# Kernel tuning notes

Measured on AMD Instinct MI355X. Metric: run time of the kernel, lower is better.

The kernel has to match this reference:

```python
import jax, jax.numpy as jnp
import numpy as np


def setup_inputs() -> dict:
    key = jax.random.key(0)
    ks = jax.random.split(key, 7)
    B, N, F, H = 128, 64, 128, 128
    s1 = 1.0 / np.sqrt(2 * N)  # torch Linear default-ish scaling
    s2 = 1.0 / np.sqrt(H)
    return {
        "agent_features": jax.random.normal(ks[0], (B, N, F), dtype=jnp.float32),
        "W1": jax.random.normal(ks[1], (2 * N, H), dtype=jnp.float32) * s1,
        "b1": jax.random.normal(ks[2], (H,), dtype=jnp.float32) * s1,
        "W2": jax.random.normal(ks[3], (H, H), dtype=jnp.float32) * s2,
        "b2": jax.random.normal(ks[4], (H,), dtype=jnp.float32) * s2,
        "w3": jax.random.normal(ks[5], (H,), dtype=jnp.float32) * s2,
        "b3": jax.random.normal(ks[6], (1,), dtype=jnp.float32) * s2,
        "mixing_weights": jnp.ones((N,), dtype=jnp.float32) / N,
    }


def reference(agent_features, W1, b1, W2, b2, w3, b3, mixing_weights):
    N = mixing_weights.shape[0]
    f = agent_features[:, :, :N]  # [B, N, N] (first num_agents features)
    # Split first Linear's weight into the i-half and j-half of the concat:
    # concat([f_i, f_j]) @ W1 == f_i @ W1[:N] + f_j @ W1[N:]
    Ai = jnp.einsum('bnf,fh->bnh', f, W1[:N])   # contribution of agent i
    Aj = jnp.einsum('bnf,fh->bnh', f, W1[N:])   # contribution of agent j
    h1 = jax.nn.relu(Ai[:, :, None, :] + Aj[:, None, :, :] + b1)  # [B,N,N,H]
    h2 = jax.nn.relu(jnp.einsum('bijh,hk->bijk', h1, W2) + b2)    # [B,N,N,H]
    correlations = jax.nn.sigmoid(jnp.einsum('bijh,h->bij', h2, w3) + b3[0])
    weights = jax.nn.softmax(mixing_weights, axis=0)
    return correlations, weights
```

## Files before the change

kernel.cpp:

```cpp
#include <hip/hip_runtime.h>
#include <hip/hip_bf16.h>


typedef __bf16 bf16x8 __attribute__((ext_vector_type(8)));
typedef float f32x4 __attribute__((ext_vector_type(4)));
typedef float f32x2 __attribute__((ext_vector_type(2)));

#define B_SZ 128
#define N_SZ 64
#define H_SZ 128

union Frag16 {
  uint4 q;
  __hip_bfloat162 h[4];
};

__global__ __launch_bounds__(256) void setup_kernel(
    const float* __restrict__ af, const float* __restrict__ W1,
    const float* __restrict__ b1, const float* __restrict__ W2,
    const float* __restrict__ mw, float* __restrict__ AiP,
    float* __restrict__ Aj, unsigned short* __restrict__ W2T,
    float* __restrict__ outw)
{
  const int blk = blockIdx.x;
  const int tid = threadIdx.x;

  if (blk < 2048) {
    __shared__ float fl[4 * 64];
    const int bn0 = blk << 2;
    fl[tid] = af[((bn0 + (tid >> 6)) << 7) + (tid & 63)];
    __syncthreads();
    const int h    = tid & 127;
    const int half = tid >> 7;
    const float* Wp = W1 + ((half << 6) << 7) + h;
    float acc0 = 0.f, acc1 = 0.f, acc2 = 0.f, acc3 = 0.f;
#pragma unroll
    for (int fq = 0; fq < 16; ++fq) {
      const float w0 = Wp[(fq * 4 + 0) << 7];
      const float w1v = Wp[(fq * 4 + 1) << 7];
      const float w2v = Wp[(fq * 4 + 2) << 7];
      const float w3v = Wp[(fq * 4 + 3) << 7];
      const float4 f0 = *(const float4*)&fl[0 * 64 + (fq << 2)];
      const float4 f1 = *(const float4*)&fl[1 * 64 + (fq << 2)];
      const float4 f2 = *(const float4*)&fl[2 * 64 + (fq << 2)];
      const float4 f3 = *(const float4*)&fl[3 * 64 + (fq << 2)];
      acc0 = fmaf(f0.x, w0, fmaf(f0.y, w1v, fmaf(f0.z, w2v, fmaf(f0.w, w3v, acc0))));
      acc1 = fmaf(f1.x, w0, fmaf(f1.y, w1v, fmaf(f1.z, w2v, fmaf(f1.w, w3v, acc1))));
      acc2 = fmaf(f2.x, w0, fmaf(f2.y, w1v, fmaf(f2.z, w2v, fmaf(f2.w, w3v, acc2))));
      acc3 = fmaf(f3.x, w0, fmaf(f3.y, w1v, fmaf(f3.z, w2v, fmaf(f3.w, w3v, acc3))));
    }
    if (half == 0) {
      const float bb = b1[h];
      AiP[((bn0 + 0) << 7) + h] = acc0 + bb;
      AiP[((bn0 + 1) << 7) + h] = acc1 + bb;
      AiP[((bn0 + 2) << 7) + h] = acc2 + bb;
      AiP[((bn0 + 3) << 7) + h] = acc3 + bb;
    } else {
      Aj[((bn0 + 0) << 7) + h] = acc0;
      Aj[((bn0 + 1) << 7) + h] = acc1;
      Aj[((bn0 + 2) << 7) + h] = acc2;
      Aj[((bn0 + 3) << 7) + h] = acc3;
    }
  } else if (blk < 2112) {
    int idx = ((blk - 2048) << 8) + tid;
    int k = idx >> 7, n = idx & 127;
    unsigned u = __float_as_uint(W2[idx]);
    u += 0x7fffu + ((u >> 16) & 1u);
    W2T[(n << 7) + k] = (unsigned short)(u >> 16);
  } else {
    if (tid < 64) {
      float v = mw[tid];
      float m = v;
      for (int off = 32; off > 0; off >>= 1) m = fmaxf(m, __shfl_xor(m, off));
      float e = expf(v - m);
      float s = e;
      for (int off = 32; off > 0; off >>= 1) s += __shfl_xor(s, off);
      outw[tid] = e / s;
    }
  }
}

__global__ __launch_bounds__(512, 4) void corr_kernel(
    const float* __restrict__ AiP, const float* __restrict__ Aj,
    const unsigned short* __restrict__ W2T,
    const float* __restrict__ b2, const float* __restrict__ w3,
    const float* __restrict__ b3, float* __restrict__ out)
{
  __shared__ __align__(16) unsigned short W2s[128 * 128];
  __shared__ __align__(16) unsigned short At[128 * 128];
  __shared__ float part[256];

  const int tid  = threadIdx.x;
  const int lane = tid & 63;
  const int wave = tid >> 6;
  const int c = lane & 15, g = lane >> 4;
  const int wm = wave & 1;
  const int wn = wave >> 1;

  const int blk = blockIdx.x;
  const int b   = blk >> 2;
  const int ip0 = (blk & 3) << 3;

  {
    const uint4* src = (const uint4*)W2T;
#pragma unroll
    for (int it = 0; it < 4; ++it) {
      const int idx = (it << 9) + tid;
      const int n = idx >> 4, e = idx & 15;
      const uint4 v = src[idx];
      *(uint4*)&W2s[(n << 7) + ((e ^ (n & 15)) << 3)] = v;
    }
  }

  f32x4 b2v[4], w3v[4];
#pragma unroll
  for (int tm = 0; tm < 4; ++tm) {
    b2v[tm] = *(const f32x4*)(b2 + (wm << 6) + (tm << 4) + (g << 2));
    w3v[tm] = *(const f32x4*)(w3 + (wm << 6) + (tm << 4) + (g << 2));
  }
  const float bias3 = b3[0];
  const f32x4 zero4 = {0.f, 0.f, 0.f, 0.f};
  const f32x2 zero2 = {0.f, 0.f};

  const float* AjB = Aj + ((b << 6) << 7);

  const int kq8 = tid & 15;
  const int rr  = tid >> 4;

  for (int t = 0; t < 8; ++t) {
    const int i0 = (ip0 + t) << 1;
    const float* AiB = AiP + (((b << 6) + i0) << 7);

#pragma unroll
    for (int pass = 0; pass < 4; ++pass) {
      const int r = (pass << 5) + rr;
      const float* arow = AiB + ((r >> 6) << 7) + (kq8 << 3);
      const float* jrow = AjB + ((r & 63) << 7) + (kq8 << 3);
      const f32x4 a0 = *(const f32x4*)arow;
      const f32x4 a1 = *(const f32x4*)(arow + 4);
      const f32x4 j0 = *(const f32x4*)jrow;
      const f32x4 j1 = *(const f32x4*)(jrow + 4);
      const f32x4 s0 = __builtin_elementwise_max(a0 + j0, zero4);
      const f32x4 s1 = __builtin_elementwise_max(a1 + j1, zero4);
      Frag16 u;
      u.h[0] = __float22bfloat162_rn(float2{s0.x, s0.y});
      u.h[1] = __float22bfloat162_rn(float2{s0.z, s0.w});
      u.h[2] = __float22bfloat162_rn(float2{s1.x, s1.y});
      u.h[3] = __float22bfloat162_rn(float2{s1.z, s1.w});
      *(uint4*)&At[(r << 7) + ((kq8 ^ (r & 15)) << 3)] = u.q;
    }

    __syncthreads();

    f32x4 acc[4][2];
#pragma unroll
    for (int tm = 0; tm < 4; ++tm) {
      acc[tm][0] = b2v[tm];
      acc[tm][1] = b2v[tm];
    }

#pragma unroll
    for (int kt = 0; kt < 4; ++kt) {
      const int es = ((kt << 2) + g) ^ c;
      bf16x8 wv[4], hv[2];
#pragma unroll
      for (int tm = 0; tm < 4; ++tm)
        wv[tm] = *(const bf16x8*)&W2s[(((wm << 6) + (tm << 4) + c) << 7) + (es << 3)];
#pragma unroll
      for (int tn = 0; tn < 2; ++tn)
        hv[tn] = *(const bf16x8*)&At[(((wn << 5) + (tn << 4) + c) << 7) + (es << 3)];
#pragma unroll
      for (int tm = 0; tm < 4; ++tm)
#pragma unroll
        for (int tn = 0; tn < 2; ++tn)
          acc[tm][tn] = __builtin_amdgcn_mfma_f32_16x16x32_bf16(
              wv[tm], hv[tn], acc[tm][tn], 0, 0, 0);
    }

    f32x2 sp0 = zero2, sp1 = zero2;
#pragma unroll
    for (int tm = 0; tm < 4; ++tm) {
      const f32x2 w3a = w3v[tm].xy, w3b = w3v[tm].zw;
      sp0 = __builtin_elementwise_max(acc[tm][0].xy, zero2) * w3a + sp0;
      sp0 = __builtin_elementwise_max(acc[tm][0].zw, zero2) * w3b + sp0;
      sp1 = __builtin_elementwise_max(acc[tm][1].xy, zero2) * w3a + sp1;
      sp1 = __builtin_elementwise_max(acc[tm][1].zw, zero2) * w3b + sp1;
    }
    float s0 = sp0.x + sp0.y;
    float s1 = sp1.x + sp1.y;
    s0 += __shfl_xor(s0, 16);
    s0 += __shfl_xor(s0, 32);
    s1 += __shfl_xor(s1, 16);
    s1 += __shfl_xor(s1, 32);
    if (g == 0) {
      part[(((wn << 5) + c) << 1) + wm]      = s0;
      part[(((wn << 5) + 16 + c) << 1) + wm] = s1;
    }

    __syncthreads();

    if (tid < 128) {
      const float2 pp = *(const float2*)&part[tid << 1];
      const float v = pp.x + pp.y + bias3;
      out[(b << 12) + (i0 << 6) + tid] = 1.f / (1.f + __expf(-v));
    }
  }
}

extern "C" void kernel_launch(void* const* d_in, const int* in_sizes, int n_in,
                              void* d_out, int out_size, void* d_ws,
                              size_t ws_size, hipStream_t stream)
{
  const float* af = (const float*)d_in[0];
  const float* W1 = (const float*)d_in[1];
  const float* b1 = (const float*)d_in[2];
  const float* W2 = (const float*)d_in[3];
  const float* b2 = (const float*)d_in[4];
  const float* w3 = (const float*)d_in[5];
  const float* b3 = (const float*)d_in[6];
  const float* mw = (const float*)d_in[7];
  float* out = (float*)d_out;

  float* AiP = (float*)d_ws;
  float* Aj  = AiP + B_SZ * N_SZ * H_SZ;
  unsigned short* W2T = (unsigned short*)(Aj + B_SZ * N_SZ * H_SZ);

  setup_kernel<<<2113, 256, 0, stream>>>(af, W1, b1, W2, mw, AiP, Aj, W2T,
                                         out + B_SZ * N_SZ * N_SZ);
  corr_kernel<<<512, 512, 0, stream>>>(AiP, Aj, W2T, b2, w3, b3, out);
}
```

Measured before the change: 103.7 us.

## Keep W2 in registers and double-buffer h1 tiles in corr kernel

The correlation kernel now holds its W2 fragments in registers, loaded once per block, instead of staging W2 in shared memory. Blocks shrink to 256 threads handling one i-row per step, and the h1 tile for the next step is built into a second shared buffer while the current one feeds the MFMAs. The grid doubles to 1024 blocks. b2 and w3 are copied by the setup kernel into a small table read each step, which trims register use at the cost of extra loads per iteration. The intent is to remove the per-block W2 shared-memory fill and LDS reads of W2, and to overlap building h1 with compute. In exchange, the 64 extra VGPRs for W2 could limit occupancy.

```diff
diff --git a/kernel.cpp b/kernel.cpp
--- a/kernel.cpp
+++ b/kernel.cpp
@@ -18,9 +18,10 @@
 __global__ __launch_bounds__(256) void setup_kernel(
     const float* __restrict__ af, const float* __restrict__ W1,
     const float* __restrict__ b1, const float* __restrict__ W2,
-    const float* __restrict__ mw, float* __restrict__ AiP,
+    const float* __restrict__ mw, const float* __restrict__ b2,
+    const float* __restrict__ w3, float* __restrict__ AiP,
     float* __restrict__ Aj, unsigned short* __restrict__ W2T,
-    float* __restrict__ outw)
+    float* __restrict__ tab, float* __restrict__ outw)
 {
   const int blk = blockIdx.x;
   const int tid = threadIdx.x;
@@ -67,7 +68,7 @@
     unsigned u = __float_as_uint(W2[idx]);
     u += 0x7fffu + ((u >> 16) & 1u);
     W2T[(n << 7) + k] = (unsigned short)(u >> 16);
-  } else {
+  } else if (blk == 2112) {
     if (tid < 64) {
       float v = mw[tid];
       float m = v;
@@ -77,18 +78,20 @@
       for (int off = 32; off > 0; off >>= 1) s += __shfl_xor(s, off);
       outw[tid] = e / s;
     }
+  } else {
+    const float v = (tid < 128) ? b2[tid] : w3[tid - 128];
+    tab[tid] = v;
+    tab[tid + 256] = v;
   }
 }
 
-__global__ __launch_bounds__(512, 4) void corr_kernel(
+__global__ __launch_bounds__(256, 4) void corr_kernel(
     const float* __restrict__ AiP, const float* __restrict__ Aj,
-    const unsigned short* __restrict__ W2T,
-    const float* __restrict__ b2, const float* __restrict__ w3,
+    const unsigned short* __restrict__ W2T, const float* __restrict__ tab,
     const float* __restrict__ b3, float* __restrict__ out)
 {
-  __shared__ __align__(16) unsigned short W2s[128 * 128];
-  __shared__ __align__(16) unsigned short At[128 * 128];
-  __shared__ float part[256];
+  __shared__ __align__(16) unsigned short S[2][64 * 128];
+  __shared__ float part[2][128];
 
   const int tid  = threadIdx.x;
   const int lane = tid & 63;
@@ -97,49 +100,34 @@
   const int wm = wave & 1;
   const int wn = wave >> 1;
 
-  const int blk = blockIdx.x;
-  const int b   = blk >> 2;
-  const int ip0 = (blk & 3) << 3;
-
-  {
-    const uint4* src = (const uint4*)W2T;
-#pragma unroll
-    for (int it = 0; it < 4; ++it) {
-      const int idx = (it << 9) + tid;
-      const int n = idx >> 4, e = idx & 15;
-      const uint4 v = src[idx];
-      *(uint4*)&W2s[(n << 7) + ((e ^ (n & 15)) << 3)] = v;
-    }
-  }
-
-  f32x4 b2v[4], w3v[4];
-#pragma unroll
-  for (int tm = 0; tm < 4; ++tm) {
-    b2v[tm] = *(const f32x4*)(b2 + (wm << 6) + (tm << 4) + (g << 2));
-    w3v[tm] = *(const f32x4*)(w3 + (wm << 6) + (tm << 4) + (g << 2));
-  }
+  const int b  = blockIdx.x >> 3;
+  const int i0 = (blockIdx.x & 7) << 3;
+
+  bf16x8 wv[4][4];
+#pragma unroll
+  for (int tm = 0; tm < 4; ++tm)
+#pragma unroll
+    for (int kt = 0; kt < 4; ++kt)
+      wv[tm][kt] = *(const bf16x8*)&W2T[(((wm << 6) + (tm << 4) + c) << 7) +
+                                        (((kt << 2) + g) << 3)];
+
+  const float* AjB = Aj + ((b << 6) << 7);
+  const int kq8 = tid & 15;
+  const int rr  = tid >> 4;
   const float bias3 = b3[0];
   const f32x4 zero4 = {0.f, 0.f, 0.f, 0.f};
   const f32x2 zero2 = {0.f, 0.f};
 
-  const float* AjB = Aj + ((b << 6) << 7);
-
-  const int kq8 = tid & 15;
-  const int rr  = tid >> 4;
-
-  for (int t = 0; t < 8; ++t) {
-    const int i0 = (ip0 + t) << 1;
-    const float* AiB = AiP + (((b << 6) + i0) << 7);
-
+  {
+    const float* AiB = AiP + (((b << 6) + i0) << 7) + (kq8 << 3);
+    const f32x4 a0 = *(const f32x4*)AiB;
+    const f32x4 a1 = *(const f32x4*)(AiB + 4);
 #pragma unroll
     for (int pass = 0; pass < 4; ++pass) {
-      const int r = (pass << 5) + rr;
-      const float* arow = AiB + ((r >> 6) << 7) + (kq8 << 3);
-      const float* jrow = AjB + ((r & 63) << 7) + (kq8 << 3);
-      const f32x4 a0 = *(const f32x4*)arow;
-      const f32x4 a1 = *(const f32x4*)(arow + 4);
-      const f32x4 j0 = *(const f32x4*)jrow;
-      const f32x4 j1 = *(const f32x4*)(jrow + 4);
+      const int r = (pass << 4) + rr;
+      const float* jr = AjB + (r << 7) + (kq8 << 3);
+      const f32x4 j0 = *(const f32x4*)jr;
+      const f32x4 j1 = *(const f32x4*)(jr + 4);
       const f32x4 s0 = __builtin_elementwise_max(a0 + j0, zero4);
       const f32x4 s1 = __builtin_elementwise_max(a1 + j1, zero4);
       Frag16 u;
@@ -147,44 +135,50 @@
       u.h[1] = __float22bfloat162_rn(float2{s0.z, s0.w});
       u.h[2] = __float22bfloat162_rn(float2{s1.x, s1.y});
       u.h[3] = __float22bfloat162_rn(float2{s1.z, s1.w});
-      *(uint4*)&At[(r << 7) + ((kq8 ^ (r & 15)) << 3)] = u.q;
-    }
-
-    __syncthreads();
+      *(uint4*)&S[0][(r << 7) + ((kq8 ^ rr) << 3)] = u.q;
+    }
+  }
+  __syncthreads();
+
+#pragma unroll 1
+  for (int t = 0; t < 8; ++t) {
+    const unsigned short* At = S[t & 1];
+    const float* tb = tab + ((t & 1) << 8);
 
     f32x4 acc[4][2];
 #pragma unroll
     for (int tm = 0; tm < 4; ++tm) {
-      acc[tm][0] = b2v[tm];
-      acc[tm][1] = b2v[tm];
+      const f32x4 b2q = *(const f32x4*)(tb + (wm << 6) + (tm << 4) + (g << 2));
+      acc[tm][0] = b2q;
+      acc[tm][1] = b2q;
     }
 
 #pragma unroll
     for (int kt = 0; kt < 4; ++kt) {
       const int es = ((kt << 2) + g) ^ c;
-      bf16x8 wv[4], hv[2];
-#pragma unroll
-      for (int tm = 0; tm < 4; ++tm)
-        wv[tm] = *(const bf16x8*)&W2s[(((wm << 6) + (tm << 4) + c) << 7) + (es << 3)];
+      bf16x8 hv[2];
 #pragma unroll
       for (int tn = 0; tn < 2; ++tn)
-        hv[tn] = *(const bf16x8*)&At[(((wn << 5) + (tn << 4) + c) << 7) + (es << 3)];
-#pragma unroll
-      for (int tm = 0; tm < 4; ++tm)
-#pragma unroll
-        for (int tn = 0; tn < 2; ++tn)
-          acc[tm][tn] = __builtin_amdgcn_mfma_f32_16x16x32_bf16(
-              wv[tm], hv[tn], acc[tm][tn], 0, 0, 0);
+        hv[tn] = *(const bf16x8*)&At[(((wn << 5) + (tn << 4) + c) << 7) +
+                                     (es << 3)];
+#pragma unroll
+      for (int tm = 0; tm < 4; ++tm) {
+        acc[tm][0] = __builtin_amdgcn_mfma_f32_16x16x32_bf16(
+            wv[tm][kt], hv[0], acc[tm][0], 0, 0, 0);
+        acc[tm][1] = __builtin_amdgcn_mfma_f32_16x16x32_bf16(
+            wv[tm][kt], hv[1], acc[tm][1], 0, 0, 0);
+      }
     }
 
     f32x2 sp0 = zero2, sp1 = zero2;
 #pragma unroll
     for (int tm = 0; tm < 4; ++tm) {
-      const f32x2 w3a = w3v[tm].xy, w3b = w3v[tm].zw;
-      sp0 = __builtin_elementwise_max(acc[tm][0].xy, zero2) * w3a + sp0;
-      sp0 = __builtin_elementwise_max(acc[tm][0].zw, zero2) * w3b + sp0;
-      sp1 = __builtin_elementwise_max(acc[tm][1].xy, zero2) * w3a + sp1;
-      sp1 = __builtin_elementwise_max(acc[tm][1].zw, zero2) * w3b + sp1;
+      const f32x4 w3q =
+          *(const f32x4*)(tb + 128 + (wm << 6) + (tm << 4) + (g << 2));
+      sp0 = __builtin_elementwise_max(acc[tm][0].xy, zero2) * w3q.xy + sp0;
+      sp0 = __builtin_elementwise_max(acc[tm][0].zw, zero2) * w3q.zw + sp0;
+      sp1 = __builtin_elementwise_max(acc[tm][1].xy, zero2) * w3q.xy + sp1;
+      sp1 = __builtin_elementwise_max(acc[tm][1].zw, zero2) * w3q.zw + sp1;
     }
     float s0 = sp0.x + sp0.y;
     float s1 = sp1.x + sp1.y;
@@ -193,16 +187,38 @@
     s1 += __shfl_xor(s1, 16);
     s1 += __shfl_xor(s1, 32);
     if (g == 0) {
-      part[(((wn << 5) + c) << 1) + wm]      = s0;
-      part[(((wn << 5) + 16 + c) << 1) + wm] = s1;
+      part[t & 1][(((wn << 5) + c) << 1) + wm]      = s0;
+      part[t & 1][(((wn << 5) + 16 + c) << 1) + wm] = s1;
+    }
+
+    if (t < 7) {
+      const float* AiB = AiP + (((b << 6) + i0 + t + 1) << 7) + (kq8 << 3);
+      const f32x4 a0 = *(const f32x4*)AiB;
+      const f32x4 a1 = *(const f32x4*)(AiB + 4);
+      unsigned short* Sn = S[(t + 1) & 1];
+#pragma unroll
+      for (int pass = 0; pass < 4; ++pass) {
+        const int r = (pass << 4) + rr;
+        const float* jr = AjB + (r << 7) + (kq8 << 3);
+        const f32x4 j0 = *(const f32x4*)jr;
+        const f32x4 j1 = *(const f32x4*)(jr + 4);
+        const f32x4 q0 = __builtin_elementwise_max(a0 + j0, zero4);
+        const f32x4 q1 = __builtin_elementwise_max(a1 + j1, zero4);
+        Frag16 u;
+        u.h[0] = __float22bfloat162_rn(float2{q0.x, q0.y});
+        u.h[1] = __float22bfloat162_rn(float2{q0.z, q0.w});
+        u.h[2] = __float22bfloat162_rn(float2{q1.x, q1.y});
+        u.h[3] = __float22bfloat162_rn(float2{q1.z, q1.w});
+        *(uint4*)&Sn[(r << 7) + ((kq8 ^ rr) << 3)] = u.q;
+      }
     }
 
     __syncthreads();
 
-    if (tid < 128) {
-      const float2 pp = *(const float2*)&part[tid << 1];
+    if (tid < 64) {
+      const float2 pp = *(const float2*)&part[t & 1][tid << 1];
       const float v = pp.x + pp.y + bias3;
-      out[(b << 12) + (i0 << 6) + tid] = 1.f / (1.f + __expf(-v));
+      out[(b << 12) + ((i0 + t) << 6) + tid] = 1.f / (1.f + __expf(-v));
     }
   }
 }
@@ -224,8 +240,10 @@
   float* AiP = (float*)d_ws;
   float* Aj  = AiP + B_SZ * N_SZ * H_SZ;
   unsigned short* W2T = (unsigned short*)(Aj + B_SZ * N_SZ * H_SZ);
-
-  setup_kernel<<<2113, 256, 0, stream>>>(af, W1, b1, W2, mw, AiP, Aj, W2T,
+  float* tab = (float*)(W2T + H_SZ * H_SZ);
+
+  setup_kernel<<<2114, 256, 0, stream>>>(af, W1, b1, W2, mw, b2, w3,
+                                         AiP, Aj, W2T, tab,
                                          out + B_SZ * N_SZ * N_SZ);
-  corr_kernel<<<512, 512, 0, stream>>>(AiP, Aj, W2T, b2, w3, b3, out);
+  corr_kernel<<<1024, 256, 0, stream>>>(AiP, Aj, W2T, tab, b3, out);
 }
```

Result: slower. 143.4 us (+38.4%).
